# Kernel optimization log

Measured on AMD Instinct MI355X. Metric: run time of the kernel, lower is better.

Reference implementation:

```python
import jax, jax.numpy as jnp
import numpy as np

B, N, D, DL, DK, DC = 4, 2048, 1024, 64, 128, 8
G_S, G_2, G_1 = 1.0, 0.5, 0.3
EPS = 1e-6

def _christoffel(dk, dl):
    # Poincare-inspired init: for k < min(dk,dl): row/col k set to 0.01, then -0.01 on the diagonal
    G = np.zeros((dk, dl, dl), np.float32)
    idx = np.arange(dl)
    for k in range(min(dk, dl)):
        G[k, k, :] = 0.01
        G[k, :, k] = 0.01
        G[k, idx, idx] -= 0.01
    return jnp.asarray(G)

def setup_inputs() -> dict:
    key = jax.random.key(0)
    ks = jax.random.split(key, 12)
    inp = {
        'x_query': jax.random.normal(ks[0], (B, D), jnp.float32),
        'z_query': 0.1 * jax.random.normal(ks[1], (B, DL), jnp.float32),
        'x_keys': jax.random.normal(ks[2], (B, N, D), jnp.float32),
        'z_keys': 0.1 * jax.random.normal(ks[3], (B, N, DL), jnp.float32),
        'W_Q': jax.random.normal(ks[4], (DK, D), jnp.float32) / np.sqrt(D),
        'W_Qz': jax.random.normal(ks[5], (DK, DL), jnp.float32) / np.sqrt(DL),
        'W_Qgamma': _christoffel(DK, DL),
        'W_K': jax.random.normal(ks[6], (DK, D), jnp.float32) / np.sqrt(D),
        'W_V': jax.random.normal(ks[7], (DK, D), jnp.float32) / np.sqrt(D),
        'W_O': jax.random.normal(ks[8], (D, DK), jnp.float32) / np.sqrt(DK),
        'W_delta': jax.random.normal(ks[9], (DC, DL), jnp.float32) / np.sqrt(DL),
        'basis_b': 0.01 * jax.random.normal(ks[10], (DC, DK, DK), jnp.float32),
        'basis_e': 0.01 * jax.random.normal(ks[11], (DC, DK, DK), jnp.float32),
        'basis_o': 0.01 * jax.random.normal(jax.random.fold_in(key, 99), (DC, DK, DK), jnp.float32),
        'log_sigma': jnp.asarray(np.log(G_S ** 2), jnp.float32),
    }
    return inp

def reference(x_query, z_query, x_keys, z_keys, W_Q, W_Qz, W_Qgamma,
              W_K, W_V, W_O, W_delta, basis_b, basis_e, basis_o, log_sigma):
    dk = W_Q.shape[0]
    # Christoffel query: linear + position + quadratic form  [B, dk]
    q = x_query @ W_Q.T + z_query @ W_Qz.T \
        + jnp.einsum('aij,bi,bj->ba', W_Qgamma, z_query, z_query)
    k = x_keys @ W_K.T            # [B, N, dk]
    v = x_keys @ W_V.T            # [B, N, dk]
    # Wilson line approx: U = I + sum_r coeff_r * (g * skew(basis_r))
    delta = z_query[:, None, :] - z_keys          # [B, N, DL]
    coeff = delta @ W_delta.T                     # [B, N, DC]
    skew = lambda b: b - jnp.swapaxes(b, -1, -2)
    basis = G_S * skew(basis_b) + G_2 * skew(basis_e) + G_1 * skew(basis_o)  # [DC, dk, dk]
    H = jnp.einsum('bnr,rij->bnij', coeff, basis)  # [B, N, dk, dk]
    kt = k + jnp.einsum('bnij,bnj->bni', H, k)     # (I + H) k
    # Conformal temperature tau = sqrt(dk) / lambda(z)
    r_sq = jnp.clip(jnp.sum(z_query ** 2, axis=-1, keepdims=True), None, 1.0 - EPS)
    lam = 2.0 / (1.0 - r_sq + EPS)                 # [B, 1]
    tau = jnp.sqrt(jnp.float32(dk)) / lam
    scores = jnp.einsum('bd,bnd->bn', q, kt) / tau
    attn = jax.nn.softmax(scores, axis=-1)
    # Area-law screening (level=0 -> sigma_eff = sigma)
    dist_sq = jnp.sum(delta ** 2, axis=-1)         # [B, N]
    area = 0.5 * lam ** 2 * dist_sq
    attn = attn * jnp.exp(-jnp.exp(log_sigma) * area)
    out = jnp.einsum('bn,bnd->bd', attn, v) @ W_O.T  # [B, D]
    return out
```

## Files before the change

### kernel.cpp

```cpp
#include <hip/hip_runtime.h>
#include <math.h>


constexpr int SC_OFF   = 0;
constexpr int WZ_OFF   = 64;
constexpr int DIST_OFF = 65600;
constexpr int AV_OFF   = 74304;
constexpr int ML_OFF   = 111168;
constexpr int PX_OFF   = 116288;
constexpr int WS_FLOATS = 640576;

__device__ __forceinline__ float wave_sum(float v) {
#pragma unroll
  for (int off = 32; off > 0; off >>= 1) v += __shfl_xor(v, off, 64);
  return v;
}

__global__ __launch_bounds__(256) void k1_prep(
    const float* __restrict__ xq, const float* __restrict__ zq,
    const float* __restrict__ zk, const float* __restrict__ WQ,
    const float* __restrict__ WQz, const float* __restrict__ Wd,
    const float* __restrict__ bb, const float* __restrict__ be,
    const float* __restrict__ bo, const float* __restrict__ WK,
    const float* __restrict__ lsig, float* __restrict__ ws,
    float* __restrict__ out) {
  const int tid = threadIdx.x;
  const int bid = blockIdx.x;
  __shared__ __align__(16) float smem[18824];

  if (bid < 36) {
    float* tmp = smem;
    float* sq  = smem + 16512;
    float* red = smem + 17024;
    float* su  = smem + 18048;
    float* szq = smem + 18560;
    float* sS1 = smem + 18816;
    float* sR2 = smem + 18820;
    const int jj = bid >> 2, dsl = bid & 3;

    float* xqs = tmp;
    for (int i = tid; i < 4096; i += 256) xqs[i] = xq[i];
    szq[tid] = zq[tid];
    __syncthreads();
    {
      const int b = tid >> 6;
      const float z = szq[tid];
      const float s1 = wave_sum(z);
      const float r2 = wave_sum(z * z);
      if ((tid & 63) == 0) { sS1[b] = s1; sR2[b] = r2; }
    }
    __syncthreads();
    {
      const int b = tid >> 7, a = tid & 127;
      const float4* w4 = (const float4*)(WQ + a * 1024);
      const float4* x0 = (const float4*)(xqs + b * 1024);
      const float4* x1 = (const float4*)(xqs + (b + 2) * 1024);
      float p0 = 0, p1 = 0;
#pragma unroll 8
      for (int c = 0; c < 256; ++c) {
        const float4 w = w4[c], xa = x0[c], xb2 = x1[c];
        p0 += w.x * xa.x + w.y * xa.y + w.z * xa.z + w.w * xa.w;
        p1 += w.x * xb2.x + w.y * xb2.y + w.z * xb2.z + w.w * xb2.w;
      }
      const float4* wz4 = (const float4*)(WQz + a * 64);
      const float4* z0 = (const float4*)(szq + b * 64);
      const float4* z1 = (const float4*)(szq + (b + 2) * 64);
#pragma unroll
      for (int c = 0; c < 16; ++c) {
        const float4 w = wz4[c], za = z0[c], zb2 = z1[c];
        p0 += w.x * za.x + w.y * za.y + w.z * za.z + w.w * za.w;
        p1 += w.x * zb2.x + w.y * zb2.y + w.z * zb2.z + w.w * zb2.w;
      }
      if (a < 64) {
        const float za = szq[b * 64 + a];
        const float zb2 = szq[(b + 2) * 64 + a];
        p0 += 0.01f * (2.0f * za * sS1[b] - sR2[b] - za * za);
        p1 += 0.01f * (2.0f * zb2 * sS1[b + 2] - sR2[b + 2] - zb2 * zb2);
      }
      sq[b * 128 + a] = p0;
      sq[(b + 2) * 128 + a] = p1;
    }
    __syncthreads();

    if (jj == 0) {
      for (int o = tid; o < 512; o += 256) su[o] = sq[o];
      __syncthreads();
    } else {
      const int r = jj - 1;
      const float4* b4 = (const float4*)(bb + r * 16384);
      const float4* e4 = (const float4*)(be + r * 16384);
      const float4* o4 = (const float4*)(bo + r * 16384);
      for (int idx = tid; idx < 4096; idx += 256) {
        const float4 vb = b4[idx], ve = e4[idx], vo = o4[idx];
        const int i = idx >> 5, col = (idx & 31) * 4;
        float* dst = tmp + i * 129 + col;
        dst[0] = vb.x + 0.5f * ve.x + 0.3f * vo.x;
        dst[1] = vb.y + 0.5f * ve.y + 0.3f * vo.y;
        dst[2] = vb.z + 0.5f * ve.z + 0.3f * vo.z;
        dst[3] = vb.w + 0.5f * ve.w + 0.3f * vo.w;
      }
      __syncthreads();
      const int j = tid & 127, h = tid >> 7;
      float a[4] = {0, 0, 0, 0};
      for (int ii = 0; ii < 64; ++ii) {
        const int i = h * 64 + ii;
        const float d = tmp[i * 129 + j] - tmp[j * 129 + i];
#pragma unroll
        for (int b = 0; b < 4; ++b) a[b] += d * sq[b * 128 + i];
      }
#pragma unroll
      for (int b = 0; b < 4; ++b) red[h * 512 + b * 128 + j] = a[b];
      __syncthreads();
      for (int o = tid; o < 512; o += 256) su[o] = red[o] + red[512 + o];
      __syncthreads();
    }

    const int d = dsl * 256 + tid;
    const float* wk = WK + d;
    float acc[4] = {0, 0, 0, 0};
#pragma unroll 8
    for (int k = 0; k < 128; ++k) {
      const float w = wk[(size_t)k * 1024];
#pragma unroll
      for (int b = 0; b < 4; ++b) acc[b] += su[b * 128 + k] * w;
    }
#pragma unroll
    for (int b = 0; b < 4; ++b)
      ws[AV_OFF + b * 9216 + jj * 1024 + d] = acc[b];
  } else if (bid < 68) {
    float* sWd = smem;
    float* szq = smem + 512;
    sWd[tid] = Wd[tid];
    sWd[256 + tid] = Wd[256 + tid];
    szq[tid] = zq[tid];
    __syncthreads();
    const int bn = (bid - 36) * 256 + tid;
    const int b = bn >> 11;
    const float4* zk4 = (const float4*)(zk + (size_t)bn * 64);
    const float* zqb = szq + b * 64;
    float wzv[8] = {0, 0, 0, 0, 0, 0, 0, 0};
    float dist = 0;
#pragma unroll
    for (int c = 0; c < 16; ++c) {
      const float4 z = zk4[c];
      const int l = c * 4;
      float d0 = zqb[l + 0] - z.x, d1 = zqb[l + 1] - z.y;
      float d2 = zqb[l + 2] - z.z, d3 = zqb[l + 3] - z.w;
      dist += d0 * d0 + d1 * d1 + d2 * d2 + d3 * d3;
#pragma unroll
      for (int r = 0; r < 8; ++r)
        wzv[r] += sWd[r * 64 + l] * z.x + sWd[r * 64 + l + 1] * z.y +
                  sWd[r * 64 + l + 2] * z.z + sWd[r * 64 + l + 3] * z.w;
    }
#pragma unroll
    for (int r = 0; r < 8; ++r) ws[WZ_OFF + bn * 8 + r] = wzv[r];
    ws[DIST_OFF + bn] = dist;
  } else {
    float* szq = smem;
    szq[tid] = zq[tid];
    __syncthreads();
    const int b = tid >> 6, l = tid & 63;
    const float z = szq[b * 64 + l];
    float r2 = wave_sum(z * z);
    float cz[8];
#pragma unroll
    for (int r = 0; r < 8; ++r) cz[r] = wave_sum(Wd[r * 64 + l] * z);
    if (l == 0) {
      r2 = fminf(r2, 1.0f - 1e-6f);
      const float lam = 2.0f / (1.0f - r2 + 1e-6f);
      ws[SC_OFF + b * 16 + 0] = lam / sqrtf(128.0f);
      ws[SC_OFF + b * 16 + 1] = expf(lsig[0]) * 0.5f * lam * lam;
#pragma unroll
      for (int r = 0; r < 8; ++r) ws[SC_OFF + b * 16 + 2 + r] = cz[r];
    }
    for (int i = tid; i < 4096; i += 256) out[i] = 0.0f;
  }
}

__global__ __launch_bounds__(256) void k2_scpx(
    const float* __restrict__ xk, float* __restrict__ ws) {
  __shared__ __align__(16) float sav[9216];
  __shared__ float pw[4096];
  __shared__ float ssc[10];
  __shared__ float sw16[16];
  __shared__ float wexp[16];
  __shared__ float wscr[16];
  const int tid = threadIdx.x;
  const int b = blockIdx.y, jb = blockIdx.x;
  const float* avg = ws + AV_OFF + b * 9216;
  for (int i = tid * 4; i < 9216; i += 1024)
    *(float4*)(sav + i) = *(const float4*)(avg + i);
  if (tid < 10) ssc[tid] = ws[SC_OFF + b * 16 + tid];
  __syncthreads();

  const int wave = tid >> 6, lane = tid & 63;
  const int nbase = jb * 16 + wave * 4;
  const float* xb = xk + ((size_t)(b * 2048 + nbase)) * 1024;

  float acc[9][4];
#pragma unroll
  for (int j = 0; j < 9; ++j)
#pragma unroll
    for (int p = 0; p < 4; ++p) acc[j][p] = 0;

#pragma unroll
  for (int c = 0; c < 4; ++c) {
    const int off = c * 256 + lane * 4;
    float4 xv[4];
#pragma unroll
    for (int p = 0; p < 4; ++p)
      xv[p] = *(const float4*)(xb + (size_t)p * 1024 + off);
#pragma unroll
    for (int j = 0; j < 9; ++j) {
      float4 a = *(const float4*)(sav + j * 1024 + off);
#pragma unroll
      for (int p = 0; p < 4; ++p)
        acc[j][p] += a.x * xv[p].x + a.y * xv[p].y + a.z * xv[p].z + a.w * xv[p].w;
    }
  }
#pragma unroll
  for (int j = 0; j < 9; ++j)
#pragma unroll
    for (int p = 0; p < 4; ++p) acc[j][p] = wave_sum(acc[j][p]);

  if (lane == 0) {
    const float it = ssc[0];
    for (int p = 0; p < 4; ++p) {
      const int bn = b * 2048 + nbase + p;
      const float* wzp = ws + WZ_OFF + bn * 8;
      float s = acc[0][p];
#pragma unroll
      for (int r = 0; r < 8; ++r) s += (ssc[2 + r] - wzp[r]) * acc[1 + r][p];
      sw16[wave * 4 + p] = s * it;
    }
  }
  __syncthreads();

  if (tid < 16) {
    float mj = sw16[0];
#pragma unroll
    for (int t = 1; t < 16; ++t) mj = fmaxf(mj, sw16[t]);
    const int n0 = jb * 16;
    wexp[tid] = expf(sw16[tid] - mj);
    wscr[tid] = expf(sw16[tid] - mj -
                     ssc[1] * ws[DIST_OFF + b * 2048 + n0 + tid]);
  }
  __syncthreads();
  if (tid == 0) {
    float mj = sw16[0];
#pragma unroll
    for (int t = 1; t < 16; ++t) mj = fmaxf(mj, sw16[t]);
    float l = 0;
#pragma unroll
    for (int t = 0; t < 16; ++t) l += wexp[t];
    ws[ML_OFF + (b * 128 + jb) * 2 + 0] = mj;
    ws[ML_OFF + (b * 128 + jb) * 2 + 1] = l;
  }

  {
    const float w0 = wscr[wave * 4 + 0], w1 = wscr[wave * 4 + 1];
    const float w2 = wscr[wave * 4 + 2], w3 = wscr[wave * 4 + 3];
    float* pwv = pw + wave * 1024;
    for (int d = lane; d < 1024; d += 64)
      pwv[d] = w0 * xb[d] + w1 * xb[1024 + d] +
               w2 * xb[2048 + d] + w3 * xb[3072 + d];
  }
  __syncthreads();
  float* px = ws + PX_OFF + ((size_t)(b * 128 + jb)) * 1024;
  for (int o = tid; o < 1024; o += 256)
    px[o] = pw[o] + pw[1024 + o] + pw[2048 + o] + pw[3072 + o];
}

__global__ __launch_bounds__(256) void k3_combout(
    const float* __restrict__ WV, const float* __restrict__ WO,
    const float* __restrict__ ws, float* __restrict__ out) {
  const int b = blockIdx.x, dsl = blockIdx.y, tid = threadIdx.x;
  __shared__ float sml[256];
  __shared__ float scj[128];
  __shared__ float part[256];
  __shared__ __align__(16) float sxb[64];
  __shared__ float sy[128];
  sml[tid] = ws[ML_OFF + b * 256 + tid];
  __syncthreads();
  float M = -3.0e38f;
#pragma unroll 8
  for (int j = 0; j < 128; ++j) M = fmaxf(M, sml[2 * j]);
  if (tid < 128) scj[tid] = expf(sml[2 * tid] - M);
  __syncthreads();
  float L = 0;
#pragma unroll 8
  for (int j = 0; j < 128; ++j) L += scj[j] * sml[2 * j + 1];
  const float rL = 1.0f / L;

  const int jq = tid >> 6, dloc = tid & 63;
  const int d0 = dsl * 64;
  const float* px = ws + PX_OFF + (size_t)b * 131072 + d0 + dloc;
  float acc = 0;
#pragma unroll 8
  for (int j = jq * 32; j < jq * 32 + 32; ++j)
    acc += scj[j] * px[(size_t)j * 1024];
  part[tid] = acc;
  __syncthreads();
  if (tid < 64)
    sxb[tid] = (part[tid] + part[64 + tid] + part[128 + tid] +
                part[192 + tid]) * rL;
  __syncthreads();

  {
    const int dk = tid >> 1, h = tid & 1;
    const float4* wv4 = (const float4*)(WV + dk * 1024 + d0 + h * 32);
    const float4* xb4 = (const float4*)(sxb + h * 32);
    float p = 0;
#pragma unroll
    for (int c = 0; c < 8; ++c) {
      const float4 w = wv4[c], x = xb4[c];
      p += w.x * x.x + w.y * x.y + w.z * x.z + w.w * x.w;
    }
    p += __shfl_xor(p, 1, 64);
    if (h == 0) sy[dk] = p;
  }
  __syncthreads();

  for (int dd = tid; dd < 1024; dd += 256) {
    const float4* wo4 = (const float4*)(WO + dd * 128);
    float a2 = 0;
#pragma unroll
    for (int c = 0; c < 32; ++c) {
      const float4 w = wo4[c];
      a2 += w.x * sy[c * 4 + 0] + w.y * sy[c * 4 + 1] +
            w.z * sy[c * 4 + 2] + w.w * sy[c * 4 + 3];
    }
    atomicAdd(&out[b * 1024 + dd], a2);
  }
}

extern "C" void kernel_launch(void* const* d_in, const int* in_sizes, int n_in,
                              void* d_out, int out_size, void* d_ws,
                              size_t ws_size, hipStream_t stream) {
  const float* xq  = (const float*)d_in[0];
  const float* zq  = (const float*)d_in[1];
  const float* xk  = (const float*)d_in[2];
  const float* zk  = (const float*)d_in[3];
  const float* WQ  = (const float*)d_in[4];
  const float* WQz = (const float*)d_in[5];
  const float* WK  = (const float*)d_in[7];
  const float* WV  = (const float*)d_in[8];
  const float* WO  = (const float*)d_in[9];
  const float* Wd  = (const float*)d_in[10];
  const float* bb  = (const float*)d_in[11];
  const float* be  = (const float*)d_in[12];
  const float* bo  = (const float*)d_in[13];
  const float* ls  = (const float*)d_in[14];
  float* ws  = (float*)d_ws;
  float* out = (float*)d_out;
  if (ws_size < (size_t)WS_FLOATS * sizeof(float)) return;

  hipLaunchKernelGGL(k1_prep, dim3(69), dim3(256), 0, stream,
                     xq, zq, zk, WQ, WQz, Wd, bb, be, bo, WK, ls, ws, out);
  hipLaunchKernelGGL(k2_scpx, dim3(128, 4), dim3(256), 0, stream, xk, ws);
  hipLaunchKernelGGL(k3_combout, dim3(4, 16), dim3(256), 0, stream,
                     WV, WO, ws, out);
}
```

Measured before the change: 189.7 us.

## Move z-key projections into score kernel and split WK projection across more blocks

Result: faster. 184.0 us (-3.0%).

```diff
diff --git a/kernel.cpp b/kernel.cpp
--- a/kernel.cpp
+++ b/kernel.cpp
@@ -2,9 +2,6 @@
 #include <math.h>
 
 
-constexpr int SC_OFF   = 0;
-constexpr int WZ_OFF   = 64;
-constexpr int DIST_OFF = 65600;
 constexpr int AV_OFF   = 74304;
 constexpr int ML_OFF   = 111168;
 constexpr int PX_OFF   = 116288;
@@ -16,181 +13,184 @@
   return v;
 }
 
-__global__ __launch_bounds__(256) void k1_prep(
+__global__ __launch_bounds__(256) void k1_uav(
     const float* __restrict__ xq, const float* __restrict__ zq,
-    const float* __restrict__ zk, const float* __restrict__ WQ,
-    const float* __restrict__ WQz, const float* __restrict__ Wd,
+    const float* __restrict__ WQ, const float* __restrict__ WQz,
     const float* __restrict__ bb, const float* __restrict__ be,
     const float* __restrict__ bo, const float* __restrict__ WK,
-    const float* __restrict__ lsig, float* __restrict__ ws,
-    float* __restrict__ out) {
+    float* __restrict__ ws, float* __restrict__ out) {
   const int tid = threadIdx.x;
   const int bid = blockIdx.x;
-  __shared__ __align__(16) float smem[18824];
-
-  if (bid < 36) {
-    float* tmp = smem;
-    float* sq  = smem + 16512;
-    float* red = smem + 17024;
-    float* su  = smem + 18048;
-    float* szq = smem + 18560;
-    float* sS1 = smem + 18816;
-    float* sR2 = smem + 18820;
-    const int jj = bid >> 2, dsl = bid & 3;
-
-    float* xqs = tmp;
-    for (int i = tid; i < 4096; i += 256) xqs[i] = xq[i];
-    szq[tid] = zq[tid];
+  if (bid == 144) {
+    for (int i = tid; i < 4096; i += 256) out[i] = 0.0f;
+    return;
+  }
+  const int jj = bid >> 4, dsl = bid & 15;
+  __shared__ __align__(16) float tmp[128 * 129];
+  __shared__ float sq[512];
+  __shared__ float red[1024];
+  __shared__ float su[512];
+  __shared__ float szq[256];
+  __shared__ float sS1[4], sR2[4];
+
+  float* xqs = tmp;
+  for (int i = tid * 4; i < 4096; i += 1024)
+    *(float4*)(xqs + i) = *(const float4*)(xq + i);
+  szq[tid] = zq[tid];
+  __syncthreads();
+  {
+    const int b = tid >> 6;
+    const float z = szq[tid];
+    const float s1 = wave_sum(z);
+    const float r2 = wave_sum(z * z);
+    if ((tid & 63) == 0) { sS1[b] = s1; sR2[b] = r2; }
+  }
+  __syncthreads();
+
+  {
+    const int b2 = tid >> 7, a = tid & 127;
+    const float4* w4 = (const float4*)(WQ + a * 1024);
+    const float4* x0 = (const float4*)(xqs + b2 * 1024);
+    const float4* x1 = (const float4*)(xqs + (b2 + 2) * 1024);
+    float p0 = 0, p1 = 0;
+#pragma unroll 8
+    for (int c = 0; c < 256; ++c) {
+      const float4 w = w4[c], xa = x0[c], xb = x1[c];
+      p0 += w.x * xa.x + w.y * xa.y + w.z * xa.z + w.w * xa.w;
+      p1 += w.x * xb.x + w.y * xb.y + w.z * xb.z + w.w * xb.w;
+    }
+    const float4* wz4 = (const float4*)(WQz + a * 64);
+    const float4* z0 = (const float4*)(szq + b2 * 64);
+    const float4* z1 = (const float4*)(szq + (b2 + 2) * 64);
+#pragma unroll
+    for (int c = 0; c < 16; ++c) {
+      const float4 w = wz4[c], za = z0[c], zb = z1[c];
+      p0 += w.x * za.x + w.y * za.y + w.z * za.z + w.w * za.w;
+      p1 += w.x * zb.x + w.y * zb.y + w.z * zb.z + w.w * zb.w;
+    }
+    if (a < 64) {
+      const float za = szq[b2 * 64 + a];
+      const float zb = szq[(b2 + 2) * 64 + a];
+      p0 += 0.01f * (2.0f * za * sS1[b2] - sR2[b2] - za * za);
+      p1 += 0.01f * (2.0f * zb * sS1[b2 + 2] - sR2[b2 + 2] - zb * zb);
+    }
+    sq[b2 * 128 + a] = p0;
+    sq[(b2 + 2) * 128 + a] = p1;
+  }
+  __syncthreads();
+
+  if (jj == 0) {
+    for (int o = tid; o < 512; o += 256) su[o] = sq[o];
+  } else {
+    const int r = jj - 1;
+    const float4* b4 = (const float4*)(bb + r * 16384);
+    const float4* e4 = (const float4*)(be + r * 16384);
+    const float4* o4 = (const float4*)(bo + r * 16384);
+    for (int idx = tid; idx < 4096; idx += 256) {
+      const float4 vb = b4[idx], ve = e4[idx], vo = o4[idx];
+      const int i = idx >> 5, col = (idx & 31) * 4;
+      float* dst = tmp + i * 129 + col;
+      dst[0] = vb.x + 0.5f * ve.x + 0.3f * vo.x;
+      dst[1] = vb.y + 0.5f * ve.y + 0.3f * vo.y;
+      dst[2] = vb.z + 0.5f * ve.z + 0.3f * vo.z;
+      dst[3] = vb.w + 0.5f * ve.w + 0.3f * vo.w;
+    }
     __syncthreads();
-    {
-      const int b = tid >> 6;
-      const float z = szq[tid];
-      const float s1 = wave_sum(z);
-      const float r2 = wave_sum(z * z);
-      if ((tid & 63) == 0) { sS1[b] = s1; sR2[b] = r2; }
-    }
+    const int j = tid & 127, h = tid >> 7;
+    float a[4] = {0, 0, 0, 0};
+    for (int ii = 0; ii < 64; ++ii) {
+      const int i = h * 64 + ii;
+      const float d = tmp[i * 129 + j] - tmp[j * 129 + i];
+#pragma unroll
+      for (int b = 0; b < 4; ++b) a[b] += d * sq[b * 128 + i];
+    }
+#pragma unroll
+    for (int b = 0; b < 4; ++b) red[h * 512 + b * 128 + j] = a[b];
     __syncthreads();
-    {
-      const int b = tid >> 7, a = tid & 127;
-      const float4* w4 = (const float4*)(WQ + a * 1024);
-      const float4* x0 = (const float4*)(xqs + b * 1024);
-      const float4* x1 = (const float4*)(xqs + (b + 2) * 1024);
-      float p0 = 0, p1 = 0;
-#pragma unroll 8
-      for (int c = 0; c < 256; ++c) {
-        const float4 w = w4[c], xa = x0[c], xb2 = x1[c];
-        p0 += w.x * xa.x + w.y * xa.y + w.z * xa.z + w.w * xa.w;
-        p1 += w.x * xb2.x + w.y * xb2.y + w.z * xb2.z + w.w * xb2.w;
-      }
-      const float4* wz4 = (const float4*)(WQz + a * 64);
-      const float4* z0 = (const float4*)(szq + b * 64);
-      const float4* z1 = (const float4*)(szq + (b + 2) * 64);
-#pragma unroll
-      for (int c = 0; c < 16; ++c) {
-        const float4 w = wz4[c], za = z0[c], zb2 = z1[c];
-        p0 += w.x * za.x + w.y * za.y + w.z * za.z + w.w * za.w;
-        p1 += w.x * zb2.x + w.y * zb2.y + w.z * zb2.z + w.w * zb2.w;
-      }
-      if (a < 64) {
-        const float za = szq[b * 64 + a];
-        const float zb2 = szq[(b + 2) * 64 + a];
-        p0 += 0.01f * (2.0f * za * sS1[b] - sR2[b] - za * za);
-        p1 += 0.01f * (2.0f * zb2 * sS1[b + 2] - sR2[b + 2] - zb2 * zb2);
-      }
-      sq[b * 128 + a] = p0;
-      sq[(b + 2) * 128 + a] = p1;
-    }
-    __syncthreads();
-
-    if (jj == 0) {
-      for (int o = tid; o < 512; o += 256) su[o] = sq[o];
-      __syncthreads();
-    } else {
-      const int r = jj - 1;
-      const float4* b4 = (const float4*)(bb + r * 16384);
-      const float4* e4 = (const float4*)(be + r * 16384);
-      const float4* o4 = (const float4*)(bo + r * 16384);
-      for (int idx = tid; idx < 4096; idx += 256) {
-        const float4 vb = b4[idx], ve = e4[idx], vo = o4[idx];
-        const int i = idx >> 5, col = (idx & 31) * 4;
-        float* dst = tmp + i * 129 + col;
-        dst[0] = vb.x + 0.5f * ve.x + 0.3f * vo.x;
-        dst[1] = vb.y + 0.5f * ve.y + 0.3f * vo.y;
-        dst[2] = vb.z + 0.5f * ve.z + 0.3f * vo.z;
-        dst[3] = vb.w + 0.5f * ve.w + 0.3f * vo.w;
-      }
-      __syncthreads();
-      const int j = tid & 127, h = tid >> 7;
-      float a[4] = {0, 0, 0, 0};
-      for (int ii = 0; ii < 64; ++ii) {
-        const int i = h * 64 + ii;
-        const float d = tmp[i * 129 + j] - tmp[j * 129 + i];
-#pragma unroll
-        for (int b = 0; b < 4; ++b) a[b] += d * sq[b * 128 + i];
-      }
-#pragma unroll
-      for (int b = 0; b < 4; ++b) red[h * 512 + b * 128 + j] = a[b];
-      __syncthreads();
-      for (int o = tid; o < 512; o += 256) su[o] = red[o] + red[512 + o];
-      __syncthreads();
-    }
-
-    const int d = dsl * 256 + tid;
-    const float* wk = WK + d;
-    float acc[4] = {0, 0, 0, 0};
-#pragma unroll 8
-    for (int k = 0; k < 128; ++k) {
-      const float w = wk[(size_t)k * 1024];
-#pragma unroll
-      for (int b = 0; b < 4; ++b) acc[b] += su[b * 128 + k] * w;
-    }
-#pragma unroll
-    for (int b = 0; b < 4; ++b)
-      ws[AV_OFF + b * 9216 + jj * 1024 + d] = acc[b];
-  } else if (bid < 68) {
-    float* sWd = smem;
-    float* szq = smem + 512;
-    sWd[tid] = Wd[tid];
-    sWd[256 + tid] = Wd[256 + tid];
-    szq[tid] = zq[tid];
-    __syncthreads();
-    const int bn = (bid - 36) * 256 + tid;
-    const int b = bn >> 11;
-    const float4* zk4 = (const float4*)(zk + (size_t)bn * 64);
-    const float* zqb = szq + b * 64;
-    float wzv[8] = {0, 0, 0, 0, 0, 0, 0, 0};
-    float dist = 0;
-#pragma unroll
-    for (int c = 0; c < 16; ++c) {
-      const float4 z = zk4[c];
-      const int l = c * 4;
-      float d0 = zqb[l + 0] - z.x, d1 = zqb[l + 1] - z.y;
-      float d2 = zqb[l + 2] - z.z, d3 = zqb[l + 3] - z.w;
-      dist += d0 * d0 + d1 * d1 + d2 * d2 + d3 * d3;
-#pragma unroll
-      for (int r = 0; r < 8; ++r)
-        wzv[r] += sWd[r * 64 + l] * z.x + sWd[r * 64 + l + 1] * z.y +
-                  sWd[r * 64 + l + 2] * z.z + sWd[r * 64 + l + 3] * z.w;
-    }
-#pragma unroll
-    for (int r = 0; r < 8; ++r) ws[WZ_OFF + bn * 8 + r] = wzv[r];
-    ws[DIST_OFF + bn] = dist;
-  } else {
-    float* szq = smem;
-    szq[tid] = zq[tid];
-    __syncthreads();
-    const int b = tid >> 6, l = tid & 63;
-    const float z = szq[b * 64 + l];
-    float r2 = wave_sum(z * z);
-    float cz[8];
-#pragma unroll
-    for (int r = 0; r < 8; ++r) cz[r] = wave_sum(Wd[r * 64 + l] * z);
-    if (l == 0) {
-      r2 = fminf(r2, 1.0f - 1e-6f);
-      const float lam = 2.0f / (1.0f - r2 + 1e-6f);
-      ws[SC_OFF + b * 16 + 0] = lam / sqrtf(128.0f);
-      ws[SC_OFF + b * 16 + 1] = expf(lsig[0]) * 0.5f * lam * lam;
-#pragma unroll
-      for (int r = 0; r < 8; ++r) ws[SC_OFF + b * 16 + 2 + r] = cz[r];
-    }
-    for (int i = tid; i < 4096; i += 256) out[i] = 0.0f;
+    for (int o = tid; o < 512; o += 256) su[o] = red[o] + red[512 + o];
+  }
+  __syncthreads();
+
+  const int kq = tid >> 6, dloc = tid & 63;
+  const int d = dsl * 64 + dloc;
+  const float* wk = WK + d;
+  float acc[4] = {0, 0, 0, 0};
+#pragma unroll 8
+  for (int k = kq * 32; k < kq * 32 + 32; ++k) {
+    const float w = wk[(size_t)k * 1024];
+#pragma unroll
+    for (int b = 0; b < 4; ++b) acc[b] += su[b * 128 + k] * w;
+  }
+#pragma unroll
+  for (int b = 0; b < 4; ++b) red[kq * 256 + b * 64 + dloc] = acc[b];
+  __syncthreads();
+  {
+    const int b = tid >> 6, dl = tid & 63;
+    const float s = red[b * 64 + dl] + red[256 + b * 64 + dl] +
+                    red[512 + b * 64 + dl] + red[768 + b * 64 + dl];
+    ws[AV_OFF + b * 9216 + jj * 1024 + dsl * 64 + dl] = s;
   }
 }
 
 __global__ __launch_bounds__(256) void k2_scpx(
-    const float* __restrict__ xk, float* __restrict__ ws) {
+    const float* __restrict__ xk, const float* __restrict__ zq,
+    const float* __restrict__ zk, const float* __restrict__ Wd,
+    const float* __restrict__ lsig, float* __restrict__ ws) {
   __shared__ __align__(16) float sav[9216];
-  __shared__ float pw[4096];
-  __shared__ float ssc[10];
+  __shared__ __align__(16) float pw[4096];
+  __shared__ __align__(16) float szk[1024];
+  __shared__ float sWd[512];
+  __shared__ float szq2[64];
+  __shared__ float swz[128];
+  __shared__ float sdist[16];
+  __shared__ float sscl[2];
+  __shared__ float scz[8];
   __shared__ float sw16[16];
   __shared__ float wexp[16];
   __shared__ float wscr[16];
   const int tid = threadIdx.x;
   const int b = blockIdx.y, jb = blockIdx.x;
+
   const float* avg = ws + AV_OFF + b * 9216;
   for (int i = tid * 4; i < 9216; i += 1024)
     *(float4*)(sav + i) = *(const float4*)(avg + i);
-  if (tid < 10) ssc[tid] = ws[SC_OFF + b * 16 + tid];
+  *(float4*)(szk + tid * 4) =
+      *(const float4*)(zk + ((size_t)(b * 2048 + jb * 16)) * 64 + tid * 4);
+  sWd[tid] = Wd[tid];
+  sWd[256 + tid] = Wd[256 + tid];
+  if (tid < 64) szq2[tid] = zq[b * 64 + tid];
+  __syncthreads();
+
+  if (tid < 64) {
+    const float z = szq2[tid];
+    float r2 = wave_sum(z * z);
+    float cz[8];
+#pragma unroll
+    for (int r = 0; r < 8; ++r) cz[r] = wave_sum(sWd[r * 64 + tid] * z);
+    if (tid == 0) {
+      r2 = fminf(r2, 1.0f - 1e-6f);
+      const float lam = 2.0f / (1.0f - r2 + 1e-6f);
+      sscl[0] = lam / sqrtf(128.0f);
+      sscl[1] = expf(lsig[0]) * 0.5f * lam * lam;
+#pragma unroll
+      for (int r = 0; r < 8; ++r) scz[r] = cz[r];
+    }
+  } else if (tid < 80) {
+    const int t = tid - 64;
+    const float* zkr = szk + t * 64;
+    float wzv[8] = {0, 0, 0, 0, 0, 0, 0, 0};
+    float dist = 0;
+    for (int l = 0; l < 64; ++l) {
+      const float zl = zkr[l];
+      const float dz = szq2[l] - zl;
+      dist += dz * dz;
+#pragma unroll
+      for (int r = 0; r < 8; ++r) wzv[r] += sWd[r * 64 + l] * zl;
+    }
+#pragma unroll
+    for (int r = 0; r < 8; ++r) swz[t * 8 + r] = wzv[r];
+    sdist[t] = dist;
+  }
   __syncthreads();
 
   const int wave = tid >> 6, lane = tid & 63;
@@ -224,14 +224,13 @@
     for (int p = 0; p < 4; ++p) acc[j][p] = wave_sum(acc[j][p]);
 
   if (lane == 0) {
-    const float it = ssc[0];
+    const float it = sscl[0];
     for (int p = 0; p < 4; ++p) {
-      const int bn = b * 2048 + nbase + p;
-      const float* wzp = ws + WZ_OFF + bn * 8;
+      const int t = wave * 4 + p;
       float s = acc[0][p];
 #pragma unroll
-      for (int r = 0; r < 8; ++r) s += (ssc[2 + r] - wzp[r]) * acc[1 + r][p];
-      sw16[wave * 4 + p] = s * it;
+      for (int r = 0; r < 8; ++r) s += (scz[r] - swz[t * 8 + r]) * acc[1 + r][p];
+      sw16[t] = s * it;
     }
   }
   __syncthreads();
@@ -240,10 +239,8 @@
     float mj = sw16[0];
 #pragma unroll
     for (int t = 1; t < 16; ++t) mj = fmaxf(mj, sw16[t]);
-    const int n0 = jb * 16;
     wexp[tid] = expf(sw16[tid] - mj);
-    wscr[tid] = expf(sw16[tid] - mj -
-                     ssc[1] * ws[DIST_OFF + b * 2048 + n0 + tid]);
+    wscr[tid] = expf(sw16[tid] - mj - sscl[1] * sdist[tid]);
   }
   __syncthreads();
   if (tid == 0) {
@@ -355,9 +352,10 @@
   float* out = (float*)d_out;
   if (ws_size < (size_t)WS_FLOATS * sizeof(float)) return;
 
-  hipLaunchKernelGGL(k1_prep, dim3(69), dim3(256), 0, stream,
-                     xq, zq, zk, WQ, WQz, Wd, bb, be, bo, WK, ls, ws, out);
-  hipLaunchKernelGGL(k2_scpx, dim3(128, 4), dim3(256), 0, stream, xk, ws);
+  hipLaunchKernelGGL(k1_uav, dim3(145), dim3(256), 0, stream,
+                     xq, zq, WQ, WQz, bb, be, bo, WK, ws, out);
+  hipLaunchKernelGGL(k2_scpx, dim3(128, 4), dim3(256), 0, stream,
+                     xk, zq, zk, Wd, ls, ws);
   hipLaunchKernelGGL(k3_combout, dim3(4, 16), dim3(256), 0, stream,
                      WV, WO, ws, out);
 }
```
